# Optimization experiments

Measured on AMD Instinct MI355X. Metric: run time of the kernel, lower is better.

The kernel has to match this reference:

```python
import jax, jax.numpy as jnp
import numpy as np

B, S, DIM = 2, 2048, 2048
H, KVH, HD = 16, 4, 128
WIN = 512
ROPE_BASE = 10000.0
EPS = 1.1920928955078125e-07  # torch F.rms_norm default eps for fp32


def setup_inputs() -> dict:
    key = jax.random.key(0)
    ks = jax.random.split(key, 6)
    kv_dim = KVH * HD
    sc = lambda fan_in: 1.0 / np.sqrt(fan_in)
    return {
        "x": jax.random.normal(ks[0], (B, S, DIM), jnp.float32),
        "Wq": jax.random.normal(ks[1], (DIM, DIM), jnp.float32) * sc(DIM),
        "Wk": jax.random.normal(ks[2], (kv_dim, DIM), jnp.float32) * sc(DIM),
        "Wv": jax.random.normal(ks[3], (kv_dim, DIM), jnp.float32) * sc(DIM),
        "Wo": jax.random.normal(ks[4], (DIM, DIM), jnp.float32) * sc(DIM),
        "q_gain": jnp.ones((H,), jnp.float32),
    }


def _rms_norm(x):
    return x * jax.lax.rsqrt(jnp.mean(x * x, axis=-1, keepdims=True) + EPS)


def _rope_tables(seqlen, dtype):
    half = HD // 2
    inv_freq = ROPE_BASE ** (-jnp.arange(0, half, dtype=jnp.float32) / half)
    freqs = jnp.arange(seqlen, dtype=jnp.float32)[:, None] * inv_freq[None, :]  # [S, HD/2]
    return jnp.cos(freqs).astype(dtype), jnp.sin(freqs).astype(dtype)


def _apply_rotary(x, cos, sin):
    # x: [B, H, S, HD]; cos/sin: [S, HD/2]
    half = x.shape[-1] // 2
    x1, x2 = x[..., :half], x[..., half:]
    c = cos[None, None, :, :]
    s = sin[None, None, :, :]
    return jnp.concatenate([x1 * c + x2 * s, -x1 * s + x2 * c], axis=-1)


def reference(x, Wq, Wk, Wv, Wo, q_gain):
    bsz, seqlen, dim = x.shape
    q = jnp.einsum("bsd,ed->bse", x, Wq).reshape(bsz, seqlen, H, HD).transpose(0, 2, 1, 3)
    k = jnp.einsum("bsd,ed->bse", x, Wk).reshape(bsz, seqlen, KVH, HD).transpose(0, 2, 1, 3)
    v = jnp.einsum("bsd,ed->bse", x, Wv).reshape(bsz, seqlen, KVH, HD).transpose(0, 2, 1, 3)

    q = _rms_norm(q)
    k = _rms_norm(k)

    cos, sin = _rope_tables(seqlen, q.dtype)
    q = _apply_rotary(q, cos, sin)
    k = _apply_rotary(k, cos, sin)

    q = q * q_gain[None, :, None, None]

    # GQA: expand kv heads to match query heads
    rep = H // KVH
    k = jnp.repeat(k, rep, axis=1)
    v = jnp.repeat(v, rep, axis=1)

    row = jnp.arange(seqlen)[:, None]
    col = jnp.arange(seqlen)[None, :]
    mask = (col <= row) & (col >= row - WIN + 1)  # [S, S]

    scale = 1.0 / np.sqrt(HD)
    scores = jnp.einsum("bhsd,bhtd->bhst", q, k) * scale
    scores = jnp.where(mask[None, None, :, :], scores, -jnp.inf)
    attn = jax.nn.softmax(scores, axis=-1)
    y = jnp.einsum("bhst,bhtd->bhsd", attn, v)  # [B, H, S, HD]

    y = y.transpose(0, 2, 1, 3).reshape(bsz, seqlen, dim)
    return jnp.einsum("bsd,ed->bse", y, Wo)
```

## Files before the change

kernel.cpp:

```cpp
#include <hip/hip_runtime.h>

#define S_LEN 2048
#define DIM   2048
#define NH    16
#define NKV   4
#define HD    128
#define WIN   512
#define BATCH 2

typedef __bf16 bf16x8 __attribute__((ext_vector_type(8)));
typedef __bf16 bf16x4 __attribute__((ext_vector_type(4)));
typedef float  f32x4  __attribute__((ext_vector_type(4)));

union U8 { bf16x8 v; bf16x4 h[2]; };

__device__ inline void async_load16(const void* g, void* l) {
  __builtin_amdgcn_global_load_lds(
      (const __attribute__((address_space(1))) unsigned int*)g,
      (__attribute__((address_space(3))) unsigned int*)l, 16, 0, 0);
}

__global__ __launch_bounds__(256) void preprocess_kernel(
    const float* __restrict__ x,
    const float* __restrict__ Wq, const float* __restrict__ Wk,
    const float* __restrict__ Wv, const float* __restrict__ Wo,
    __bf16* __restrict__ xb, __bf16* __restrict__ wqkv, __bf16* __restrict__ wob,
    float* __restrict__ cosT, float* __restrict__ sinT) {
  const int blk = blockIdx.x, tid = threadIdx.x;
  if (blk < 8192) {
    int i = blk * 256 + tid;
    float4 v = ((const float4*)x)[i];
    bf16x4 o;
    o[0] = (__bf16)v.x; o[1] = (__bf16)v.y; o[2] = (__bf16)v.z; o[3] = (__bf16)v.w;
    ((bf16x4*)xb)[i] = o;
  } else if (blk < 18432) {
    int i = (blk - 8192) * 256 + tid;
    int orow = i >> 9, c = i & 511;
    const float* src;
    __bf16* dst;
    long soff;
    if (orow < 2048) {
      int n = orow & 127;
      int sr = (orow & ~127) + ((n >> 5) << 4) + (n & 15) + (((n >> 4) & 1) << 6);
      src = Wq; soff = (long)sr * 512 + c; dst = wqkv + (long)orow * 2048;
    } else if (orow < 2560) {
      int lr = orow - 2048, n = lr & 127;
      int sr = (lr & ~127) + ((n >> 5) << 4) + (n & 15) + (((n >> 4) & 1) << 6);
      src = Wk; soff = (long)sr * 512 + c; dst = wqkv + (long)orow * 2048;
    } else if (orow < 3072) {
      src = Wv; soff = (long)(orow - 2560) * 512 + c; dst = wqkv + (long)orow * 2048;
    } else {
      src = Wo; soff = (long)(orow - 3072) * 512 + c; dst = wob + (long)(orow - 3072) * 2048;
    }
    float4 v = ((const float4*)src)[soff];
    bf16x4 o;
    o[0] = (__bf16)v.x; o[1] = (__bf16)v.y; o[2] = (__bf16)v.z; o[3] = (__bf16)v.w;
    ((bf16x4*)dst)[c] = o;
  } else {
    int idx = (blk - 18432) * 256 + tid;
    int s = idx >> 6, d = idx & 63;
    float f = (float)s * powf(10000.f, -(float)d * (1.f / 64.f));
    float sn, cs;
    sincosf(f, &sn, &cs);
    cosT[idx] = cs;
    sinT[idx] = sn;
  }
}

__global__ __launch_bounds__(512, 2) void gemm_bt(
    const __bf16* __restrict__ A, const __bf16* __restrict__ Bt,
    float* __restrict__ C, int M, int N, int K) {
  extern __shared__ char smem[];
  const int NT = K >> 6;
  const int t = threadIdx.x;
  const int wid = t >> 6, lane = t & 63;
  const int quad = lane >> 4, l15 = lane & 15;
  const int wr = wid >> 2, wc = wid & 3;
  const long m0 = (long)blockIdx.x * 128, n0 = (long)blockIdx.y * 256;

  const int srw = (wid << 3) + (lane >> 3);
  const int c8 = (lane & 7) ^ ((lane >> 3) & 7);
  const __bf16* ag = A + (m0 + srw) * (long)K + c8 * 8;
  const __bf16* bg = Bt + (n0 + srw) * (long)K + c8 * 8;

  auto stageA = [&](int buf, int j, int kt) {
    async_load16(ag + (long)(j << 6) * K + (long)kt * 64,
                 smem + buf * 49152 + j * 8192 + t * 16);
  };
  auto stageB = [&](int buf, int j, int kt) {
    async_load16(bg + (long)(j << 6) * K + (long)kt * 64,
                 smem + buf * 49152 + 16384 + j * 8192 + t * 16);
  };

  const int swz = (l15 & 7) << 4;
  const int col0 = (quad * 16) ^ swz;
  const int col1 = (64 + quad * 16) ^ swz;

  f32x4 zero = {0.f, 0.f, 0.f, 0.f};
  f32x4 acc[4][4];
#pragma unroll
  for (int i = 0; i < 4; ++i)
#pragma unroll
    for (int j = 0; j < 4; ++j) acc[i][j] = zero;

#pragma unroll
  for (int j = 0; j < 2; ++j) stageA(0, j, 0);
#pragma unroll
  for (int j = 0; j < 4; ++j) stageB(0, j, 0);
#pragma unroll
  for (int j = 0; j < 2; ++j) stageA(1, j, 1);

  auto tile = [&](const int buf, const int tt) {
    const char* As = smem + buf * 49152;
    const char* Bs = smem + buf * 49152 + 16384;
    if (tt + 1 < NT) {
#pragma unroll
      for (int j = 0; j < 4; ++j) stageB(buf ^ 1, j, tt + 1);
      asm volatile("s_waitcnt vmcnt(6)" ::: "memory");
    } else {
      asm volatile("s_waitcnt vmcnt(0)" ::: "memory");
    }
    __builtin_amdgcn_s_barrier();
    bf16x8 af[4][2], bf[2][2];
#pragma unroll
    for (int i = 0; i < 4; ++i) {
      const int rb = (wr * 64 + i * 16 + l15) * 128;
      af[i][0] = *(const bf16x8*)(As + rb + col0);
      af[i][1] = *(const bf16x8*)(As + rb + col1);
    }
#pragma unroll
    for (int j = 0; j < 2; ++j) {
      const int rb = (wc * 64 + j * 16 + l15) * 128;
      bf[j][0] = *(const bf16x8*)(Bs + rb + col0);
      bf[j][1] = *(const bf16x8*)(Bs + rb + col1);
    }
    asm volatile("s_waitcnt lgkmcnt(0)" ::: "memory");
    __builtin_amdgcn_sched_barrier(0);
    __builtin_amdgcn_s_setprio(1);
#pragma unroll
    for (int kk = 0; kk < 2; ++kk)
#pragma unroll
      for (int i = 0; i < 4; ++i)
#pragma unroll
        for (int j = 0; j < 2; ++j)
          acc[i][j] = __builtin_amdgcn_mfma_f32_16x16x32_bf16(af[i][kk], bf[j][kk],
                                                              acc[i][j], 0, 0, 0);
    __builtin_amdgcn_s_setprio(0);
    __builtin_amdgcn_s_barrier();
#pragma unroll
    for (int j = 0; j < 2; ++j) {
      const int rb = (wc * 64 + (j + 2) * 16 + l15) * 128;
      bf[j][0] = *(const bf16x8*)(Bs + rb + col0);
      bf[j][1] = *(const bf16x8*)(Bs + rb + col1);
    }
    if (tt + 2 < NT) {
#pragma unroll
      for (int j = 0; j < 2; ++j) stageA(buf, j, tt + 2);
    }
    asm volatile("s_waitcnt lgkmcnt(0)" ::: "memory");
    __builtin_amdgcn_sched_barrier(0);
    __builtin_amdgcn_s_setprio(1);
#pragma unroll
    for (int kk = 0; kk < 2; ++kk)
#pragma unroll
      for (int i = 0; i < 4; ++i)
#pragma unroll
        for (int j = 0; j < 2; ++j)
          acc[i][j + 2] = __builtin_amdgcn_mfma_f32_16x16x32_bf16(af[i][kk], bf[j][kk],
                                                                  acc[i][j + 2], 0, 0, 0);
    __builtin_amdgcn_s_setprio(0);
    __builtin_amdgcn_s_barrier();
  };

  for (int tt = 0; tt < NT; tt += 2) {
    tile(0, tt);
    tile(1, tt + 1);
  }

#pragma unroll
  for (int i = 0; i < 4; ++i)
#pragma unroll
    for (int j = 0; j < 4; ++j)
#pragma unroll
      for (int r = 0; r < 4; ++r)
        C[(m0 + wr * 64 + i * 16 + quad * 4 + r) * (long)N + n0 + wc * 64 + j * 16 + l15] =
            acc[i][j][r];
}

__global__ __launch_bounds__(512, 2) void gemm_qkv(
    const __bf16* __restrict__ A, const __bf16* __restrict__ Bt,
    const float* __restrict__ gain,
    const float* __restrict__ cosT, const float* __restrict__ sinT,
    __bf16* __restrict__ Qo, __bf16* __restrict__ Ko, __bf16* __restrict__ Vt) {
  extern __shared__ char smem[];
  constexpr int K = 2048;
  constexpr int NT = 32;
  const int t = threadIdx.x;
  const int wid = t >> 6, lane = t & 63;
  const int quad = lane >> 4, l15 = lane & 15;
  const int wr = wid >> 2, wc = wid & 3;
  const long m0 = (long)blockIdx.x * 128;
  const long n0 = (long)blockIdx.y * 256;

  const int srw = (wid << 3) + (lane >> 3);
  const int c8 = (lane & 7) ^ ((lane >> 3) & 7);
  const __bf16* ag = A + (m0 + srw) * (long)K + c8 * 8;
  const __bf16* bg = Bt + (n0 + srw) * (long)K + c8 * 8;

  auto stageA = [&](int j, int kt) {
    async_load16(ag + (long)(j << 6) * K + (long)kt * 64,
                 smem + j * 8192 + t * 16);
  };
  auto stageB = [&](int buf, int j, int kt) {
    async_load16(bg + (long)(j << 6) * K + (long)kt * 64,
                 smem + 16384 + buf * 32768 + j * 8192 + t * 16);
  };

  const int swz = (l15 & 7) << 4;
  const int col0 = (quad * 16) ^ swz;
  const int col1 = (64 + quad * 16) ^ swz;

  f32x4 zero = {0.f, 0.f, 0.f, 0.f};
  f32x4 acc[4][4];
#pragma unroll
  for (int i = 0; i < 4; ++i)
#pragma unroll
    for (int j = 0; j < 4; ++j) acc[i][j] = zero;

#pragma unroll
  for (int j = 0; j < 4; ++j) stageB(0, j, 0);
#pragma unroll
  for (int j = 0; j < 2; ++j) stageA(j, 0);

  auto tile = [&](const int buf, const int tt) {
    const char* As = smem;
    const char* Bs = smem + 16384 + buf * 32768;
    if (tt + 1 < NT) {
#pragma unroll
      for (int j = 0; j < 4; ++j) stageB(buf ^ 1, j, tt + 1);
      asm volatile("s_waitcnt vmcnt(4)" ::: "memory");
    } else {
      asm volatile("s_waitcnt vmcnt(0)" ::: "memory");
    }
    __builtin_amdgcn_s_barrier();
    bf16x8 af[4][2], bf[2][2];
#pragma unroll
    for (int i = 0; i < 4; ++i) {
      const int rb = (wr * 64 + i * 16 + l15) * 128;
      af[i][0] = *(const bf16x8*)(As + rb + col0);
      af[i][1] = *(const bf16x8*)(As + rb + col1);
    }
#pragma unroll
    for (int j = 0; j < 2; ++j) {
      const int rb = (wc * 64 + j * 16 + l15) * 128;
      bf[j][0] = *(const bf16x8*)(Bs + rb + col0);
      bf[j][1] = *(const bf16x8*)(Bs + rb + col1);
    }
    asm volatile("s_waitcnt lgkmcnt(0)" ::: "memory");
    __builtin_amdgcn_sched_barrier(0);
    __builtin_amdgcn_s_setprio(1);
#pragma unroll
    for (int kk = 0; kk < 2; ++kk)
#pragma unroll
      for (int i = 0; i < 4; ++i)
#pragma unroll
        for (int j = 0; j < 2; ++j)
          acc[i][j] = __builtin_amdgcn_mfma_f32_16x16x32_bf16(af[i][kk], bf[j][kk],
                                                              acc[i][j], 0, 0, 0);
    __builtin_amdgcn_s_setprio(0);
    __builtin_amdgcn_s_barrier();
    if (tt + 1 < NT) {
#pragma unroll
      for (int j = 0; j < 2; ++j) stageA(j, tt + 1);
    }
#pragma unroll
    for (int j = 0; j < 2; ++j) {
      const int rb = (wc * 64 + (j + 2) * 16 + l15) * 128;
      bf[j][0] = *(const bf16x8*)(Bs + rb + col0);
      bf[j][1] = *(const bf16x8*)(Bs + rb + col1);
    }
    asm volatile("s_waitcnt lgkmcnt(0)" ::: "memory");
    __builtin_amdgcn_sched_barrier(0);
    __builtin_amdgcn_s_setprio(1);
#pragma unroll
    for (int kk = 0; kk < 2; ++kk)
#pragma unroll
      for (int i = 0; i < 4; ++i)
#pragma unroll
        for (int j = 0; j < 2; ++j)
          acc[i][j + 2] = __builtin_amdgcn_mfma_f32_16x16x32_bf16(af[i][kk], bf[j][kk],
                                                                  acc[i][j + 2], 0, 0, 0);
    __builtin_amdgcn_s_setprio(0);
    __builtin_amdgcn_s_barrier();
  };

  for (int tt = 0; tt < NT; tt += 2) {
    tile(0, tt);
    tile(1, tt + 1);
  }

  const int by = blockIdx.y;
  const int srow0 = (int)(m0 & 2047);
  const int bb = (int)(m0 >> 11);
  const int brow = (wc & 1) << 6;

  if (by >= 10) {
    const int kvh = (by - 10) * 2 + (wc >> 1);
    __bf16* Vb = Vt + ((long)(bb * NKV + kvh)) * HD * S_LEN;
#pragma unroll
    for (int i = 0; i < 4; ++i)
#pragma unroll
      for (int j = 0; j < 4; ++j) {
        const int d = brow + j * 16 + l15;
        const int s0 = srow0 + wr * 64 + i * 16 + quad * 4;
        bf16x4 o;
#pragma unroll
        for (int r = 0; r < 4; ++r) o[r] = (__bf16)acc[i][j][r];
        *(bf16x4*)(Vb + (long)d * S_LEN + s0) = o;
      }
  } else {
    float* sums = (float*)smem;
#pragma unroll
    for (int i = 0; i < 4; ++i)
#pragma unroll
      for (int r = 0; r < 4; ++r) {
        float t2 = acc[i][0][r] * acc[i][0][r] + acc[i][1][r] * acc[i][1][r] +
                   acc[i][2][r] * acc[i][2][r] + acc[i][3][r] * acc[i][3][r];
#pragma unroll
        for (int off = 1; off < 16; off <<= 1) t2 += __shfl_xor(t2, off, 64);
        if (l15 == 0) sums[(wr * 64 + i * 16 + quad * 4 + r) * 4 + wc] = t2;
      }
    __syncthreads();

    float g;
    __bf16* base;
    if (by < 8) {
      const int h = by * 2 + (wc >> 1);
      g = gain[h] * 0.08838834764831845f;
      base = Qo + ((long)(bb * NH + h)) * S_LEN * HD;
    } else {
      const int h = (by - 8) * 2 + (wc >> 1);
      g = 1.f;
      base = Ko + ((long)(bb * NKV + h)) * S_LEN * HD;
    }
#pragma unroll
    for (int i = 0; i < 4; ++i)
#pragma unroll
      for (int r = 0; r < 4; ++r) {
        const int lrow = wr * 64 + i * 16 + quad * 4 + r;
        const int srow = srow0 + lrow;
        const float rs = rsqrtf((sums[lrow * 4 + (wc & 2)] + sums[lrow * 4 + (wc & 2) + 1]) *
                                    (1.f / 128.f) +
                                1.1920928955078125e-07f);
#pragma unroll
        for (int a = 0; a < 2; ++a) {
          const int dlow = ((wc & 1) << 5) + a * 16 + l15;
          const float cv = cosT[srow * 64 + dlow];
          const float sv = sinT[srow * 64 + dlow];
          const float x1 = acc[i][2 * a][r] * rs;
          const float x2 = acc[i][2 * a + 1][r] * rs;
          base[(long)srow * HD + brow + (2 * a) * 16 + l15] = (__bf16)((x1 * cv + x2 * sv) * g);
          base[(long)srow * HD + brow + (2 * a + 1) * 16 + l15] = (__bf16)((-x1 * sv + x2 * cv) * g);
        }
      }
  }
}

__global__ __launch_bounds__(512, 4) void attn_kernel(
    const __bf16* __restrict__ Q,
    const __bf16* __restrict__ K,
    const __bf16* __restrict__ Vt,
    const float* __restrict__ gain,
    __bf16* __restrict__ Y) {
  __shared__ __bf16 Ks[64 * 128];
  __shared__ __bf16 Vs[128 * 64];
  __shared__ __bf16 Ps[8][16 * 64];

  const int t = threadIdx.x;
  const int wid = t >> 6, lane = t & 63;
  const int quad = lane >> 4, l15 = lane & 15;
  const int qt_blk = 15 - blockIdx.x;
  const int h = blockIdx.y, b = blockIdx.z;
  const int kv = h >> 2;
  const int t0 = qt_blk * 128;
  const int r0 = t0 + wid * 16;

  const __bf16* Qb = Q + ((long)(b * NH + h)) * S_LEN * HD;
  const __bf16* Kb = K + ((long)(b * NKV + kv)) * S_LEN * HD;
  const __bf16* Vb = Vt + ((long)(b * NKV + kv)) * HD * S_LEN;
  const float M = 11.3137085f * fabsf(gain[h]);

  bf16x8 qf[4];
#pragma unroll
  for (int c = 0; c < 4; ++c)
    qf[c] = *(const bf16x8*)(Qb + (long)(r0 + l15) * HD + c * 32 + quad * 8);

  f32x4 zero = {0.f, 0.f, 0.f, 0.f};
  f32x4 acc[8];
#pragma unroll
  for (int d = 0; d < 8; ++d) acc[d] = zero;
  float lac = 0.f;

  int ksrc[2], vsrc[2];
#pragma unroll
  for (int j = 0; j < 2; ++j) {
    int kr = j * 32 + (t >> 4);
    ksrc[j] = kr * HD + (((t & 15) ^ (kr & 15)) << 3);
    int vd = j * 64 + (t >> 3);
    vsrc[j] = vd * S_LEN + (((t & 7) ^ (vd & 7)) << 3);
  }

  const int kstart = (t0 >= WIN) ? (t0 - WIN) : 0;
  const int ntiles = (t0 + 128 - kstart) >> 6;

  for (int it = 0; it < ntiles; ++it) {
    const int kt = kstart + it * 64;
#pragma unroll
    for (int j = 0; j < 2; ++j) {
      async_load16(Kb + (long)kt * HD + ksrc[j], (char*)Ks + j * 8192 + t * 16);
      async_load16(Vb + kt + vsrc[j], (char*)Vs + j * 8192 + t * 16);
    }
    __syncthreads();

    if (kt <= r0 + 15 && kt + 63 >= r0 - (WIN - 1)) {
#pragma unroll
      for (int kti = 0; kti < 4; ++kti) {
        bf16x8 kf[4];
#pragma unroll
        for (int c = 0; c < 4; ++c)
          kf[c] = *(const bf16x8*)(Ks + (kti * 16 + l15) * 128 +
                                   ((((c << 2) + quad) ^ l15) << 3));
        f32x4 sc = zero;
#pragma unroll
        for (int c = 0; c < 4; ++c)
          sc = __builtin_amdgcn_mfma_f32_16x16x32_bf16(kf[c], qf[c], sc, 0, 0, 0);
        const int qg = r0 + l15;
        const int kbase = kt + kti * 16 + quad * 4;
        bf16x4 pv;
#pragma unroll
        for (int r = 0; r < 4; ++r) {
          int key = kbase + r;
          float p = (key <= qg && key >= qg - (WIN - 1)) ? __expf(sc[r] - M) : 0.f;
          lac += p;
          pv[r] = (__bf16)p;
        }
        const int cb = kti * 4 + quad;
        *(bf16x4*)(&Ps[wid][l15 * 64 + ((cb ^ l15) << 2)]) = pv;
      }
      bf16x8 pf[2];
#pragma unroll
      for (int kc = 0; kc < 2; ++kc) {
        U8 u;
        u.h[0] = *(const bf16x4*)(&Ps[wid][l15 * 64 + (((kc * 8 + quad * 2) ^ l15) << 2)]);
        u.h[1] = *(const bf16x4*)(&Ps[wid][l15 * 64 + (((kc * 8 + quad * 2 + 1) ^ l15) << 2)]);
        pf[kc] = u.v;
      }
#pragma unroll
      for (int dt = 0; dt < 8; ++dt)
#pragma unroll
        for (int kc = 0; kc < 2; ++kc) {
          bf16x8 vf = *(const bf16x8*)(Vs + (dt * 16 + l15) * 64 +
                                       ((((kc << 2) + quad) ^ (l15 & 7)) << 3));
          acc[dt] = __builtin_amdgcn_mfma_f32_16x16x32_bf16(pf[kc], vf, acc[dt], 0, 0, 0);
        }
    }
    __syncthreads();
  }

  float s = lac;
  s += __shfl_xor(s, 16, 64);
  s += __shfl_xor(s, 32, 64);
  __bf16* Yb = Y + ((long)b * S_LEN) * DIM + h * HD;
#pragma unroll
  for (int r = 0; r < 4; ++r) {
    const int row = quad * 4 + r;
    float il = 1.f / __shfl(s, row, 64);
#pragma unroll
    for (int dt = 0; dt < 8; ++dt)
      Yb[(long)(r0 + row) * DIM + dt * 16 + l15] = (__bf16)(acc[dt][r] * il);
  }
}

extern "C" void kernel_launch(void* const* d_in, const int* in_sizes, int n_in,
                              void* d_out, int out_size, void* d_ws, size_t ws_size,
                              hipStream_t stream) {
  (void)in_sizes; (void)n_in; (void)out_size; (void)ws_size;
  const float* x  = (const float*)d_in[0];
  const float* Wq = (const float*)d_in[1];
  const float* Wk = (const float*)d_in[2];
  const float* Wv = (const float*)d_in[3];
  const float* Wo = (const float*)d_in[4];
  const float* qg = (const float*)d_in[5];
  float* out = (float*)d_out;

  char* ws = (char*)d_ws;
  size_t off = 0;
  auto alloc = [&](size_t bytes) -> void* {
    void* p = ws + off;
    off += (bytes + 255) & ~(size_t)255;
    return p;
  };
  __bf16* xb   = (__bf16*)alloc(8388608ull * 2);
  __bf16* wqkv = (__bf16*)alloc(3072ull * 2048 * 2);
  __bf16* wob  = (__bf16*)alloc(2048ull * 2048 * 2);
  __bf16* qo   = (__bf16*)alloc((size_t)BATCH * NH * S_LEN * HD * 2);
  __bf16* ko   = (__bf16*)alloc((size_t)BATCH * NKV * S_LEN * HD * 2);
  __bf16* vt   = (__bf16*)alloc((size_t)BATCH * NKV * HD * S_LEN * 2);
  float*  cosT = (float*)alloc(2048ull * 64 * 4);
  float*  sinT = (float*)alloc(2048ull * 64 * 4);
  __bf16* yb   = xb;

  (void)hipFuncSetAttribute((const void*)gemm_bt,
                            hipFuncAttributeMaxDynamicSharedMemorySize, 98304);
  (void)hipFuncSetAttribute((const void*)gemm_qkv,
                            hipFuncAttributeMaxDynamicSharedMemorySize, 81920);

  preprocess_kernel<<<18944, 256, 0, stream>>>(x, Wq, Wk, Wv, Wo, xb, wqkv, wob,
                                               cosT, sinT);
  gemm_qkv<<<dim3(32, 12), 512, 81920, stream>>>(xb, wqkv, qg, cosT, sinT, qo, ko, vt);
  attn_kernel<<<dim3(16, 16, 2), 512, 0, stream>>>(qo, ko, vt, qg, yb);
  gemm_bt<<<dim3(32, 8), 512, 98304, stream>>>(yb, wob, out, 4096, 2048, 2048);
}
```

Baseline: 252.9 us.

## Retile QKV GEMM to 256x192 and move RMS-norm/RoPE to separate kernel

New measurement: 248.0 us. Within noise of the previous version (-1.9%).

```diff
diff --git a/kernel.cpp b/kernel.cpp
--- a/kernel.cpp
+++ b/kernel.cpp
@@ -189,9 +189,8 @@
 
 __global__ __launch_bounds__(512, 2) void gemm_qkv(
     const __bf16* __restrict__ A, const __bf16* __restrict__ Bt,
-    const float* __restrict__ gain,
-    const float* __restrict__ cosT, const float* __restrict__ sinT,
-    __bf16* __restrict__ Qo, __bf16* __restrict__ Ko, __bf16* __restrict__ Vt) {
+    float* __restrict__ qkraw,
+    __bf16* __restrict__ Vt) {
   extern __shared__ char smem[];
   constexpr int K = 2048;
   constexpr int NT = 32;
@@ -199,21 +198,21 @@
   const int wid = t >> 6, lane = t & 63;
   const int quad = lane >> 4, l15 = lane & 15;
   const int wr = wid >> 2, wc = wid & 3;
-  const long m0 = (long)blockIdx.x * 128;
-  const long n0 = (long)blockIdx.y * 256;
+  const long m0 = (long)blockIdx.x * 256;
+  const long n0 = (long)blockIdx.y * 192;
 
   const int srw = (wid << 3) + (lane >> 3);
   const int c8 = (lane & 7) ^ ((lane >> 3) & 7);
   const __bf16* ag = A + (m0 + srw) * (long)K + c8 * 8;
   const __bf16* bg = Bt + (n0 + srw) * (long)K + c8 * 8;
 
-  auto stageA = [&](int j, int kt) {
+  auto stageA = [&](int buf, int j, int kt) {
     async_load16(ag + (long)(j << 6) * K + (long)kt * 64,
-                 smem + j * 8192 + t * 16);
+                 smem + buf * 32768 + j * 8192 + t * 16);
   };
   auto stageB = [&](int buf, int j, int kt) {
     async_load16(bg + (long)(j << 6) * K + (long)kt * 64,
-                 smem + 16384 + buf * 32768 + j * 8192 + t * 16);
+                 smem + 65536 + buf * 24576 + j * 8192 + t * 16);
   };
 
   const int swz = (l15 & 7) << 4;
@@ -221,76 +220,84 @@
   const int col1 = (64 + quad * 16) ^ swz;
 
   f32x4 zero = {0.f, 0.f, 0.f, 0.f};
-  f32x4 acc[4][4];
-#pragma unroll
-  for (int i = 0; i < 4; ++i)
-#pragma unroll
-    for (int j = 0; j < 4; ++j) acc[i][j] = zero;
-
-#pragma unroll
-  for (int j = 0; j < 4; ++j) stageB(0, j, 0);
-#pragma unroll
-  for (int j = 0; j < 2; ++j) stageA(j, 0);
+  f32x4 acc[8][3];
+#pragma unroll
+  for (int i = 0; i < 8; ++i)
+#pragma unroll
+    for (int j = 0; j < 3; ++j) acc[i][j] = zero;
+
+#pragma unroll
+  for (int j = 0; j < 3; ++j) stageB(0, j, 0);
+#pragma unroll
+  for (int j = 0; j < 4; ++j) stageA(0, j, 0);
+#pragma unroll
+  for (int j = 0; j < 3; ++j) stageB(1, j, 1);
 
   auto tile = [&](const int buf, const int tt) {
-    const char* As = smem;
-    const char* Bs = smem + 16384 + buf * 32768;
+    const char* As = smem + buf * 32768;
+    const char* Bs = smem + 65536 + buf * 24576;
     if (tt + 1 < NT) {
 #pragma unroll
-      for (int j = 0; j < 4; ++j) stageB(buf ^ 1, j, tt + 1);
-      asm volatile("s_waitcnt vmcnt(4)" ::: "memory");
+      for (int j = 0; j < 4; ++j) stageA(buf ^ 1, j, tt + 1);
+      asm volatile("s_waitcnt vmcnt(7)" ::: "memory");
     } else {
       asm volatile("s_waitcnt vmcnt(0)" ::: "memory");
     }
     __builtin_amdgcn_s_barrier();
-    bf16x8 af[4][2], bf[2][2];
-#pragma unroll
-    for (int i = 0; i < 4; ++i) {
-      const int rb = (wr * 64 + i * 16 + l15) * 128;
-      af[i][0] = *(const bf16x8*)(As + rb + col0);
-      af[i][1] = *(const bf16x8*)(As + rb + col1);
-    }
-#pragma unroll
-    for (int j = 0; j < 2; ++j) {
-      const int rb = (wc * 64 + j * 16 + l15) * 128;
+    bf16x8 bf[3][2];
+#pragma unroll
+    for (int j = 0; j < 3; ++j) {
+      const int rb = (wc * 48 + j * 16 + l15) * 128;
       bf[j][0] = *(const bf16x8*)(Bs + rb + col0);
       bf[j][1] = *(const bf16x8*)(Bs + rb + col1);
     }
-    asm volatile("s_waitcnt lgkmcnt(0)" ::: "memory");
-    __builtin_amdgcn_sched_barrier(0);
-    __builtin_amdgcn_s_setprio(1);
-#pragma unroll
-    for (int kk = 0; kk < 2; ++kk)
-#pragma unroll
-      for (int i = 0; i < 4; ++i)
-#pragma unroll
-        for (int j = 0; j < 2; ++j)
-          acc[i][j] = __builtin_amdgcn_mfma_f32_16x16x32_bf16(af[i][kk], bf[j][kk],
-                                                              acc[i][j], 0, 0, 0);
-    __builtin_amdgcn_s_setprio(0);
+    {
+      bf16x8 afl[4][2];
+#pragma unroll
+      for (int i = 0; i < 4; ++i) {
+        const int rb = (wr * 128 + i * 16 + l15) * 128;
+        afl[i][0] = *(const bf16x8*)(As + rb + col0);
+        afl[i][1] = *(const bf16x8*)(As + rb + col1);
+      }
+      asm volatile("s_waitcnt lgkmcnt(0)" ::: "memory");
+      __builtin_amdgcn_sched_barrier(0);
+      __builtin_amdgcn_s_setprio(1);
+#pragma unroll
+      for (int kk = 0; kk < 2; ++kk)
+#pragma unroll
+        for (int i = 0; i < 4; ++i)
+#pragma unroll
+          for (int j = 0; j < 3; ++j)
+            acc[i][j] = __builtin_amdgcn_mfma_f32_16x16x32_bf16(afl[i][kk], bf[j][kk],
+                                                                acc[i][j], 0, 0, 0);
+      __builtin_amdgcn_s_setprio(0);
+    }
     __builtin_amdgcn_s_barrier();
-    if (tt + 1 < NT) {
-#pragma unroll
-      for (int j = 0; j < 2; ++j) stageA(j, tt + 1);
-    }
-#pragma unroll
-    for (int j = 0; j < 2; ++j) {
-      const int rb = (wc * 64 + (j + 2) * 16 + l15) * 128;
-      bf[j][0] = *(const bf16x8*)(Bs + rb + col0);
-      bf[j][1] = *(const bf16x8*)(Bs + rb + col1);
-    }
-    asm volatile("s_waitcnt lgkmcnt(0)" ::: "memory");
-    __builtin_amdgcn_sched_barrier(0);
-    __builtin_amdgcn_s_setprio(1);
-#pragma unroll
-    for (int kk = 0; kk < 2; ++kk)
-#pragma unroll
-      for (int i = 0; i < 4; ++i)
-#pragma unroll
-        for (int j = 0; j < 2; ++j)
-          acc[i][j + 2] = __builtin_amdgcn_mfma_f32_16x16x32_bf16(af[i][kk], bf[j][kk],
-                                                                  acc[i][j + 2], 0, 0, 0);
-    __builtin_amdgcn_s_setprio(0);
+    {
+      bf16x8 afh[4][2];
+#pragma unroll
+      for (int i = 0; i < 4; ++i) {
+        const int rb = (wr * 128 + (i + 4) * 16 + l15) * 128;
+        afh[i][0] = *(const bf16x8*)(As + rb + col0);
+        afh[i][1] = *(const bf16x8*)(As + rb + col1);
+      }
+      if (tt + 2 < NT) {
+#pragma unroll
+        for (int j = 0; j < 3; ++j) stageB(buf, j, tt + 2);
+      }
+      asm volatile("s_waitcnt lgkmcnt(0)" ::: "memory");
+      __builtin_amdgcn_sched_barrier(0);
+      __builtin_amdgcn_s_setprio(1);
+#pragma unroll
+      for (int kk = 0; kk < 2; ++kk)
+#pragma unroll
+        for (int i = 0; i < 4; ++i)
+#pragma unroll
+          for (int j = 0; j < 3; ++j)
+            acc[i + 4][j] = __builtin_amdgcn_mfma_f32_16x16x32_bf16(afh[i][kk], bf[j][kk],
+                                                                    acc[i + 4][j], 0, 0, 0);
+      __builtin_amdgcn_s_setprio(0);
+    }
     __builtin_amdgcn_s_barrier();
   };
 
@@ -299,70 +306,68 @@
     tile(1, tt + 1);
   }
 
-  const int by = blockIdx.y;
   const int srow0 = (int)(m0 & 2047);
   const int bb = (int)(m0 >> 11);
-  const int brow = (wc & 1) << 6;
-
-  if (by >= 10) {
-    const int kvh = (by - 10) * 2 + (wc >> 1);
-    __bf16* Vb = Vt + ((long)(bb * NKV + kvh)) * HD * S_LEN;
-#pragma unroll
-    for (int i = 0; i < 4; ++i)
-#pragma unroll
-      for (int j = 0; j < 4; ++j) {
-        const int d = brow + j * 16 + l15;
-        const int s0 = srow0 + wr * 64 + i * 16 + quad * 4;
+#pragma unroll
+  for (int j = 0; j < 3; ++j) {
+    const int n = (int)n0 + wc * 48 + j * 16 + l15;
+    if (n < 2560) {
+#pragma unroll
+      for (int i = 0; i < 8; ++i) {
+        const long row = m0 + wr * 128 + i * 16 + quad * 4;
+#pragma unroll
+        for (int r = 0; r < 4; ++r) qkraw[(row + r) * 2560 + n] = acc[i][j][r];
+      }
+    } else {
+      const int d = (n - 2560) & 127, kvh = (n - 2560) >> 7;
+      __bf16* Vb = Vt + ((long)(bb * NKV + kvh)) * HD * S_LEN;
+#pragma unroll
+      for (int i = 0; i < 8; ++i) {
+        const int s0 = srow0 + wr * 128 + i * 16 + quad * 4;
         bf16x4 o;
 #pragma unroll
         for (int r = 0; r < 4; ++r) o[r] = (__bf16)acc[i][j][r];
         *(bf16x4*)(Vb + (long)d * S_LEN + s0) = o;
       }
-  } else {
-    float* sums = (float*)smem;
-#pragma unroll
-    for (int i = 0; i < 4; ++i)
-#pragma unroll
-      for (int r = 0; r < 4; ++r) {
-        float t2 = acc[i][0][r] * acc[i][0][r] + acc[i][1][r] * acc[i][1][r] +
-                   acc[i][2][r] * acc[i][2][r] + acc[i][3][r] * acc[i][3][r];
-#pragma unroll
-        for (int off = 1; off < 16; off <<= 1) t2 += __shfl_xor(t2, off, 64);
-        if (l15 == 0) sums[(wr * 64 + i * 16 + quad * 4 + r) * 4 + wc] = t2;
-      }
-    __syncthreads();
-
+    }
+  }
+}
+
+__global__ __launch_bounds__(256) void rms_rope(
+    const float* __restrict__ qkraw, const float* __restrict__ gain,
+    const float* __restrict__ cosT, const float* __restrict__ sinT,
+    __bf16* __restrict__ Qo, __bf16* __restrict__ Ko) {
+  const int m = blockIdx.x;
+  const int wid = threadIdx.x >> 6, lane = threadIdx.x & 63;
+  const int u = lane & 15, a = lane >> 4;
+  const int srow = m & 2047, bb = m >> 11;
+  const int c = a * 32 + u;
+  const int dlow = a * 16 + u;
+  const float cv = cosT[srow * 64 + dlow];
+  const float sv = sinT[srow * 64 + dlow];
+  const float* rowp = qkraw + (long)m * 2560;
+#pragma unroll
+  for (int hh = 0; hh < 5; ++hh) {
+    const int head = wid * 5 + hh;
+    const float* hp = rowp + head * 128;
+    const float x1 = hp[c];
+    const float x2 = hp[c + 16];
+    float ss = x1 * x1 + x2 * x2;
+#pragma unroll
+    for (int off = 1; off < 64; off <<= 1) ss += __shfl_xor(ss, off, 64);
+    const float rs = rsqrtf(ss * (1.f / 128.f) + 1.1920928955078125e-07f);
     float g;
     __bf16* base;
-    if (by < 8) {
-      const int h = by * 2 + (wc >> 1);
-      g = gain[h] * 0.08838834764831845f;
-      base = Qo + ((long)(bb * NH + h)) * S_LEN * HD;
+    if (head < NH) {
+      g = gain[head] * 0.08838834764831845f;
+      base = Qo + ((long)(bb * NH + head)) * S_LEN * HD;
     } else {
-      const int h = (by - 8) * 2 + (wc >> 1);
       g = 1.f;
-      base = Ko + ((long)(bb * NKV + h)) * S_LEN * HD;
-    }
-#pragma unroll
-    for (int i = 0; i < 4; ++i)
-#pragma unroll
-      for (int r = 0; r < 4; ++r) {
-        const int lrow = wr * 64 + i * 16 + quad * 4 + r;
-        const int srow = srow0 + lrow;
-        const float rs = rsqrtf((sums[lrow * 4 + (wc & 2)] + sums[lrow * 4 + (wc & 2) + 1]) *
-                                    (1.f / 128.f) +
-                                1.1920928955078125e-07f);
-#pragma unroll
-        for (int a = 0; a < 2; ++a) {
-          const int dlow = ((wc & 1) << 5) + a * 16 + l15;
-          const float cv = cosT[srow * 64 + dlow];
-          const float sv = sinT[srow * 64 + dlow];
-          const float x1 = acc[i][2 * a][r] * rs;
-          const float x2 = acc[i][2 * a + 1][r] * rs;
-          base[(long)srow * HD + brow + (2 * a) * 16 + l15] = (__bf16)((x1 * cv + x2 * sv) * g);
-          base[(long)srow * HD + brow + (2 * a + 1) * 16 + l15] = (__bf16)((-x1 * sv + x2 * cv) * g);
-        }
-      }
+      base = Ko + ((long)(bb * NKV + (head - NH))) * S_LEN * HD;
+    }
+    const float y1 = x1 * rs, y2 = x2 * rs;
+    base[(long)srow * HD + c] = (__bf16)((y1 * cv + y2 * sv) * g);
+    base[(long)srow * HD + c + 16] = (__bf16)((-y1 * sv + y2 * cv) * g);
   }
 }
 
@@ -508,16 +513,18 @@
   __bf16* vt   = (__bf16*)alloc((size_t)BATCH * NKV * HD * S_LEN * 2);
   float*  cosT = (float*)alloc(2048ull * 64 * 4);
   float*  sinT = (float*)alloc(2048ull * 64 * 4);
+  float*  qkraw = (float*)alloc(4096ull * 2560 * 4);
   __bf16* yb   = xb;
 
   (void)hipFuncSetAttribute((const void*)gemm_bt,
                             hipFuncAttributeMaxDynamicSharedMemorySize, 98304);
   (void)hipFuncSetAttribute((const void*)gemm_qkv,
-                            hipFuncAttributeMaxDynamicSharedMemorySize, 81920);
+                            hipFuncAttributeMaxDynamicSharedMemorySize, 114688);
 
   preprocess_kernel<<<18944, 256, 0, stream>>>(x, Wq, Wk, Wv, Wo, xb, wqkv, wob,
                                                cosT, sinT);
-  gemm_qkv<<<dim3(32, 12), 512, 81920, stream>>>(xb, wqkv, qg, cosT, sinT, qo, ko, vt);
+  gemm_qkv<<<dim3(16, 16), 512, 114688, stream>>>(xb, wqkv, qkraw, vt);
+  rms_rope<<<4096, 256, 0, stream>>>(qkraw, qg, cosT, sinT, qo, ko);
   attn_kernel<<<dim3(16, 16, 2), 512, 0, stream>>>(qo, ko, vt, qg, yb);
   gemm_bt<<<dim3(32, 8), 512, 98304, stream>>>(yb, wob, out, 4096, 2048, 2048);
 }
```
